# Kernel tuning notes

Hardware: AMD Instinct MI355X
Metric: run time of the kernel (lower is better)

## Reference

```python
import jax, jax.numpy as jnp
import numpy as np

HEADS = 8
DIM_HEAD = 64
EPS_NORM = 1e-5

def chan_layer_norm(x, g, b):
    # normalize over channel dim (axis=1), biased variance, eps inside sqrt
    mean = jnp.mean(x, axis=1, keepdims=True)
    var = jnp.mean((x - mean) ** 2, axis=1, keepdims=True)
    return (x - mean) / jnp.sqrt(var + EPS_NORM) * g + b

def l2norm(x):
    # F.normalize over dim=1 with eps=1e-12
    n = jnp.linalg.norm(x, axis=1, keepdims=True)
    return x / jnp.maximum(n, 1e-12)

def conv1x1(w, x):
    # w: (out_c, in_c), x: (b, in_c, h, w)
    return jnp.einsum('oc,bchw->bohw', w, x)

def setup_inputs() -> dict:
    key = jax.random.key(0)
    ks = jax.random.split(key, 8)
    dim, inner = 256, HEADS * DIM_HEAD
    B, H, W = 8, 64, 64
    inp = {
        'query_source': jax.random.normal(ks[0], (B, dim, H, W), jnp.float32),
        'context': jax.random.normal(ks[1], (B, dim, H, W), jnp.float32),
        'cn_g': jnp.ones((1, dim, 1, 1), jnp.float32),
        'cn_b': jnp.zeros((1, dim, 1, 1), jnp.float32),
        'qn_g': jnp.ones((1, dim, 1, 1), jnp.float32),
        'qn_b': jnp.zeros((1, dim, 1, 1), jnp.float32),
        'on_g': jnp.ones((1, dim, 1, 1), jnp.float32),
        'on_b': jnp.zeros((1, dim, 1, 1), jnp.float32),
        'w_kv': jax.random.normal(ks[2], (inner * 2, dim), jnp.float32) * (dim ** -0.5),
        'w_q': jax.random.normal(ks[3], (inner, dim), jnp.float32) * (dim ** -0.5),
        'w_out': jax.random.normal(ks[4], (dim, inner), jnp.float32) * (inner ** -0.5),
        'gamma': jnp.full((1,), 0.5, jnp.float32),  # nonzero so output depends on attention path
    }
    return inp

def reference(query_source, context, cn_g, cn_b, qn_g, qn_b, on_g, on_b, w_kv, w_q, w_out, gamma):
    B, C, Hq, Wq = query_source.shape
    _, _, Hc, Wc = context.shape
    kh = int(Hc ** 0.5)  # height_top_k default
    kw = int(Wc ** 0.5)  # width_top_k default

    ctx = chan_layer_norm(context, cn_g, cn_b)
    qs = chan_layer_norm(query_source, qn_g, qn_b)

    kv = conv1x1(w_kv, ctx)                      # (B, 2*inner, Hc, Wc)
    k, v = jnp.split(kv, 2, axis=1)
    q = conv1x1(w_q, qs)                         # (B, inner, Hq, Wq)

    def fold(x):
        b, hc, h, w = x.shape
        return x.reshape(b, HEADS, DIM_HEAD, h, w).reshape(b * HEADS, DIM_HEAD, h, w)
    q, k, v = fold(q), fold(k), fold(v)

    q, k = l2norm(q), l2norm(k)

    if kh < Hc or kw < Wc:
        k_abs = jnp.abs(k)
        q_probe = q.sum(axis=(2, 3))             # (bh, c)
        if kh < Hc:
            score_r = jnp.einsum('bc,bch->bh', q_probe, k_abs.sum(axis=3))
            idx_h = jax.lax.top_k(score_r, kh)[1]            # (bh, kh)
            idx = idx_h[:, None, :, None]
            k = jnp.take_along_axis(k, idx, axis=2)
            v = jnp.take_along_axis(v, idx, axis=2)
        if kw < Wc:
            score_c = jnp.einsum('bc,bcw->bw', q_probe, k_abs.sum(axis=2))
            idx_w = jax.lax.top_k(score_c, kw)[1]            # (bh, kw)
            idx = idx_w[:, None, None, :]
            k = jnp.take_along_axis(k, idx, axis=3)
            v = jnp.take_along_axis(v, idx, axis=3)

    def flat(x):  # (bh, c, h, w) -> (bh, h*w, c)
        bh, c = x.shape[:2]
        return x.reshape(bh, c, -1).transpose(0, 2, 1)
    qf, kf, vf = flat(q), flat(k), flat(v)

    sim = jnp.einsum('bid,bjd->bij', qf, kf)     # (bh, Hq*Wq, kh*kw)
    attn = jax.nn.softmax(sim, axis=-1)
    out = jnp.einsum('bij,bjd->bid', attn, vf)   # (bh, Hq*Wq, c)

    out = out.reshape(B, HEADS, Hq, Wq, DIM_HEAD)
    out = out.transpose(0, 1, 4, 2, 3).reshape(B, HEADS * DIM_HEAD, Hq, Wq)
    out = conv1x1(w_out, out)
    out = chan_layer_norm(out, on_g, on_b)
    return gamma * out + query_source
```

## Files before the change

kernel.cpp:

```cpp
#include <hip/hip_runtime.h>
#include <hip/hip_bf16.h>

#define BB 8
#define CDIM 256
#define PP 4096
#define NHEADS 8
#define DHEAD 64
#define INNER 512
#define NBH 64

using bf16 = __hip_bfloat16;
typedef short short8 __attribute__((ext_vector_type(8)));
typedef float f32x4 __attribute__((ext_vector_type(4)));
typedef unsigned short u16;

__device__ __forceinline__ float b2f(bf16 x) { return __bfloat162float(x); }
__device__ __forceinline__ bf16 f2b(float x) { return __float2bfloat16(x); }

__device__ __forceinline__ u16 f2h(float x) {
    union { float f; unsigned u; } c; c.f = x;
    unsigned r = c.u + 0x7FFF + ((c.u >> 16) & 1);
    return (u16)(r >> 16);
}
__device__ __forceinline__ float h2f(u16 h) {
    union { float f; unsigned u; } c; c.u = ((unsigned)h) << 16;
    return c.f;
}

__device__ __forceinline__ int sw(int row, int kb) {
    return row * 128 + (kb ^ ((row & 7) << 4));
}

__device__ __forceinline__ void gload16(const void* g, void* lds) {
    __builtin_amdgcn_global_load_lds((const __attribute__((address_space(1))) void*)g,
                                     (__attribute__((address_space(3))) void*)lds, 16, 0, 0);
}

__device__ __forceinline__ void remap(int& o0, int& p0, int& b) {
    unsigned GS = gridDim.x;
    unsigned h = (blockIdx.z * gridDim.y + blockIdx.y) * GS + blockIdx.x;
    unsigned xc = h & 7, m = h >> 3;
    unsigned g = (m / GS) * 8 + xc;
    o0 = (int)(m % GS) * 64;
    p0 = (int)(g & 63) * 64;
    b  = (int)(g >> 6);
}

__global__ __launch_bounds__(256) void wsplit_kernel(const float* __restrict__ W,
                                                     u16* __restrict__ WH,
                                                     u16* __restrict__ WL) {
    int i = blockIdx.x * 256 + threadIdx.x;
    float v = W[i];
    u16 hb = f2h(v);
    WH[i] = hb;
    if (WL) WL[i] = f2h(v - h2f(hb));
}

__global__ __launch_bounds__(256) void ln_split_kernel(const float* __restrict__ x,
                                                       const float* __restrict__ g,
                                                       const float* __restrict__ bb,
                                                       u16* __restrict__ XH,
                                                       u16* __restrict__ XL) {
    int b = blockIdx.y;
    int p0 = blockIdx.x * 64;
    int tid = threadIdx.x;
    int px = tid & 63, cg = tid >> 6;
    __shared__ float red_s[4][64], red_q[4][64], meanv[64], rstdv[64];

    const float* xb = x + (size_t)b * CDIM * PP + p0 + px;
    float s = 0.f, sq = 0.f;
#pragma unroll 8
    for (int i = 0; i < 64; ++i) {
        float v = xb[(size_t)(cg * 64 + i) * PP];
        s += v; sq += v * v;
    }
    red_s[cg][px] = s; red_q[cg][px] = sq;
    __syncthreads();
    if (tid < 64) {
        float ts = red_s[0][tid] + red_s[1][tid] + red_s[2][tid] + red_s[3][tid];
        float tq = red_q[0][tid] + red_q[1][tid] + red_q[2][tid] + red_q[3][tid];
        float mean = ts * (1.f / CDIM);
        float var  = tq * (1.f / CDIM) - mean * mean;
        meanv[tid] = mean;
        rstdv[tid] = rsqrtf(var + 1e-5f);
    }
    __syncthreads();
    float mean = meanv[px], rstd = rstdv[px];
    size_t orow = ((size_t)b * PP + p0 + px) * CDIM;
    for (int c0 = cg * 64; c0 < cg * 64 + 64; c0 += 8) {
        short8 hv, lv;
#pragma unroll
        for (int j = 0; j < 8; ++j) {
            int c = c0 + j;
            float v = xb[(size_t)c * PP];
            float n = (v - mean) * rstd * g[c] + bb[c];
            u16 hb = f2h(n);
            hv[j] = (short)hb;
            lv[j] = (short)f2h(n - h2f(hb));
        }
        *(short8*)(XH + orow + c0) = hv;
        *(short8*)(XL + orow + c0) = lv;
    }
}

__global__ __launch_bounds__(256) void mfma_qkv_kernel(const u16* __restrict__ WH,
                                                       const u16* __restrict__ WL,
                                                       const u16* __restrict__ XH,
                                                       const u16* __restrict__ XL,
                                                       u16* __restrict__ dstA,
                                                       u16* __restrict__ dstB,
                                                       int Kdim, int norm_below, int mode,
                                                       float* __restrict__ part_out,
                                                       const float* __restrict__ q_probe) {
    __shared__ alignas(16) char sm[32768];
    __shared__ float red[16][64];
    __shared__ float rinv[64];
    __shared__ float qp_s[64];
    char* AH = sm;
    char* AL = sm + 8192;
    char* BH = sm + 16384;
    char* BL = sm + 24576;
    float* C = (float*)sm;

    int o0, p0, b;
    remap(o0, p0, b);
    int tid = threadIdx.x;
    int l = tid & 63, w = tid >> 6;
    int wm = w >> 1, wn = w & 1;
    int lr = l & 15, lk = l >> 4;
    int r8 = l >> 3;
    int kswz = ((l & 7) * 16) ^ (r8 << 4);

    bool donorm = (o0 < norm_below);
    if (mode == 0 && donorm && tid < 64)
        qp_s[tid] = q_probe[(size_t)(b * NHEADS + (o0 >> 6)) * 64 + tid];

    f32x4 acc[2][2] = {};

    for (int k0 = 0; k0 < Kdim; k0 += 64) {
#pragma unroll
        for (int j = 0; j < 2; ++j) {
            int rb = w * 16 + j * 8;
            int row = rb + r8;
            size_t aoff = ((size_t)(o0 + row) * Kdim + k0) * 2 + kswz;
            size_t boff = (((size_t)b * PP + p0 + row) * Kdim + k0) * 2 + kswz;
            gload16((const char*)WH + aoff, AH + rb * 128);
            gload16((const char*)WL + aoff, AL + rb * 128);
            gload16((const char*)XH + boff, BH + rb * 128);
            gload16((const char*)XL + boff, BL + rb * 128);
        }
        __syncthreads();
#pragma unroll
        for (int kk = 0; kk < 2; ++kk) {
            int kb = kk * 64 + lk * 16;
            short8 ah[2], al[2], bh[2], bl[2];
#pragma unroll
            for (int f = 0; f < 2; ++f) {
                ah[f] = *(short8*)(AH + sw(wm * 32 + f * 16 + lr, kb));
                al[f] = *(short8*)(AL + sw(wm * 32 + f * 16 + lr, kb));
                bh[f] = *(short8*)(BH + sw(wn * 32 + f * 16 + lr, kb));
                bl[f] = *(short8*)(BL + sw(wn * 32 + f * 16 + lr, kb));
            }
#pragma unroll
            for (int fm = 0; fm < 2; ++fm)
#pragma unroll
                for (int fn = 0; fn < 2; ++fn) {
                    acc[fm][fn] = __builtin_amdgcn_mfma_f32_16x16x32_bf16(ah[fm], bh[fn], acc[fm][fn], 0, 0, 0);
                    acc[fm][fn] = __builtin_amdgcn_mfma_f32_16x16x32_bf16(ah[fm], bl[fn], acc[fm][fn], 0, 0, 0);
                    acc[fm][fn] = __builtin_amdgcn_mfma_f32_16x16x32_bf16(al[fm], bh[fn], acc[fm][fn], 0, 0, 0);
                }
        }
        __syncthreads();
    }

#pragma unroll
    for (int fm = 0; fm < 2; ++fm)
#pragma unroll
        for (int fn = 0; fn < 2; ++fn)
#pragma unroll
            for (int r = 0; r < 4; ++r)
                C[(wm * 32 + fm * 16 + lk * 4 + r) * 65 + wn * 32 + fn * 16 + lr] = acc[fm][fn][r];
    __syncthreads();

    int tx = tid & 15, ty = tid >> 4;
    float a2[4][4];
#pragma unroll
    for (int i = 0; i < 4; ++i)
#pragma unroll
        for (int j = 0; j < 4; ++j)
            a2[i][j] = C[(ty * 4 + i) * 65 + tx * 4 + j];

    if (donorm) {
#pragma unroll
        for (int j = 0; j < 4; ++j) {
            float sj = 0.f;
#pragma unroll
            for (int i = 0; i < 4; ++i) sj += a2[i][j] * a2[i][j];
            red[ty][tx * 4 + j] = sj;
        }
        __syncthreads();
        if (tid < 64) {
            float s = 0.f;
#pragma unroll
            for (int yy = 0; yy < 16; ++yy) s += red[yy][tid];
            rinv[tid] = 1.f / fmaxf(sqrtf(s), 1e-12f);
        }
        __syncthreads();
#pragma unroll
        for (int i = 0; i < 4; ++i)
#pragma unroll
            for (int j = 0; j < 4; ++j)
                a2[i][j] *= rinv[tx * 4 + j];
    }

    if (mode == 1) {
        int p_l = tid & 63, og = tid >> 6;
        float rv = rinv[p_l];
        u16* qrow = dstA + ((size_t)(b * NHEADS + (o0 >> 6)) * PP + p0 + p_l) * 64 + og * 16;
        short8 s0, s1;
#pragma unroll
        for (int i = 0; i < 8; ++i) s0[i] = (short)f2h(C[(og * 16 + i) * 65 + p_l] * rv);
#pragma unroll
        for (int i = 0; i < 8; ++i) s1[i] = (short)f2h(C[(og * 16 + 8 + i) * 65 + p_l] * rv);
        *(short8*)qrow = s0;
        *(short8*)(qrow + 8) = s1;
    } else {
        int oo = donorm ? o0 : (o0 - norm_below);
        u16* dest = donorm ? dstA : dstB;
#pragma unroll
        for (int i = 0; i < 4; ++i) {
            int oc = oo + ty * 4 + i;
            int bh = b * NHEADS + (oc >> 6);
            int d  = oc & 63;
            u16* drow = dest + ((size_t)bh * DHEAD + d) * PP + p0;
#pragma unroll
            for (int j = 0; j < 4; ++j) drow[tx * 4 + j] = f2h(a2[i][j]);
        }
    }

    if (donorm) {
        int bh = b * NHEADS + (o0 >> 6);
        int h  = p0 >> 6;
        if (mode == 0) {
            float cj[4];
#pragma unroll
            for (int j = 0; j < 4; ++j) {
                float s = 0.f;
#pragma unroll
                for (int i = 0; i < 4; ++i) s += qp_s[ty * 4 + i] * fabsf(a2[i][j]);
                cj[j] = s;
            }
            __syncthreads();
#pragma unroll
            for (int j = 0; j < 4; ++j) red[ty][tx * 4 + j] = cj[j];
            __syncthreads();
            if (tid < 64) {
                float s = 0.f;
#pragma unroll
                for (int t = 0; t < 16; ++t) s += red[t][tid];
                part_out[((size_t)bh * 64 + h) * 64 + tid] = s;
            }
        } else {
            float part[4];
#pragma unroll
            for (int i = 0; i < 4; ++i) {
                float s = 0.f;
#pragma unroll
                for (int j = 0; j < 4; ++j) s += a2[i][j];
                part[i] = s;
            }
            __syncthreads();
#pragma unroll
            for (int i = 0; i < 4; ++i) red[tx][ty * 4 + i] = part[i];
            __syncthreads();
            if (tid < 64) {
                float s = 0.f;
#pragma unroll
                for (int t = 0; t < 16; ++t) s += red[t][tid];
                part_out[((size_t)bh * 64 + h) * 64 + tid] = s;
            }
        }
    }
}

__global__ __launch_bounds__(64) void qreduce_kernel(const float* __restrict__ part,
                                                     float* __restrict__ q_probe) {
    int bh = blockIdx.x, d = threadIdx.x;
    float s = 0.f;
    for (int h = 0; h < 64; ++h) s += part[((size_t)bh * 64 + h) * 64 + d];
    q_probe[(size_t)bh * 64 + d] = s;
}

__global__ __launch_bounds__(256) void select_gather_kernel(const float* __restrict__ colpart,
                                                            const u16* __restrict__ kn,
                                                            const u16* __restrict__ vs,
                                                            u16* __restrict__ k_sel,
                                                            u16* __restrict__ v_selt) {
    int bh = blockIdx.x;
    int tid = threadIdx.x;
    __shared__ float M[64][65];
    __shared__ int selh[8], selw[8];
    for (int i = tid; i < 4096; i += 256) M[i >> 6][i & 63] = colpart[(size_t)bh * 4096 + i];
    __syncthreads();
    if (tid < 128) {
        int isCol = tid >> 6;
        int x = tid & 63;
        float sv = 0.f;
        if (isCol) { for (int h = 0; h < 64; ++h) sv += M[h][x]; }
        else       { for (int w = 0; w < 64; ++w) sv += M[x][w]; }
        float v = sv;
        for (int it = 0; it < 8; ++it) {
            float bv = v; int bi = x;
#pragma unroll
            for (int off = 32; off; off >>= 1) {
                float ov = __shfl_xor(bv, off);
                int   oi = __shfl_xor(bi, off);
                if (ov > bv || (ov == bv && oi < bi)) { bv = ov; bi = oi; }
            }
            if (x == 0) { if (isCol) selw[it] = bi; else selh[it] = bi; }
            if (x == bi) v = -3.4e38f;
        }
    }
    __syncthreads();
    for (int idx = tid; idx < 4096; idx += 256) {
        int j = idx >> 6, d = idx & 63;
        int p = selh[j >> 3] * 64 + selw[j & 7];
        u16 kv = kn[((size_t)bh * 64 + d) * PP + p];
        u16 vv = vs[((size_t)bh * 64 + d) * PP + p];
        k_sel[(size_t)bh * 4096 + j * 64 + d]  = kv;
        v_selt[(size_t)bh * 4096 + d * 64 + j] = vv;
    }
}

__global__ __launch_bounds__(256) void attn_mfma_kernel(const u16* __restrict__ qt,
                                                        const u16* __restrict__ ksel,
                                                        const u16* __restrict__ vselt,
                                                        u16* __restrict__ attn_t) {
    __shared__ alignas(16) char AQ[8192];
    __shared__ alignas(16) char BK[8192];
    __shared__ alignas(16) char BV[8192];
    __shared__ float SIM[64 * 68];
    int bh = blockIdx.y;
    int p0 = blockIdx.x * 64;
    int b = bh >> 3, h = bh & 7;
    int tid = threadIdx.x;
    int l = tid & 63, w = tid >> 6;
    int wm = w >> 1, wn = w & 1;
    int lr = l & 15, lk = l >> 4;
    int r8 = l >> 3;
    int kswz = ((l & 7) * 16) ^ (r8 << 4);

#pragma unroll
    for (int j = 0; j < 2; ++j) {
        int rb = w * 16 + j * 8;
        int row = rb + r8;
        gload16((const char*)qt + ((size_t)bh * PP + p0 + row) * 128 + kswz, AQ + rb * 128);
        gload16((const char*)ksel + ((size_t)bh * 64 + row) * 128 + kswz, BK + rb * 128);
        gload16((const char*)vselt + ((size_t)bh * 64 + row) * 128 + kswz, BV + rb * 128);
    }
    __syncthreads();

    f32x4 acc[2][2] = {};
#pragma unroll
    for (int kk = 0; kk < 2; ++kk) {
        int kb = kk * 64 + lk * 16;
        short8 av[2], bv[2];
#pragma unroll
        for (int f = 0; f < 2; ++f) {
            av[f] = *(short8*)(AQ + sw(wm * 32 + f * 16 + lr, kb));
            bv[f] = *(short8*)(BK + sw(wn * 32 + f * 16 + lr, kb));
        }
#pragma unroll
        for (int fm = 0; fm < 2; ++fm)
#pragma unroll
            for (int fn = 0; fn < 2; ++fn)
                acc[fm][fn] = __builtin_amdgcn_mfma_f32_16x16x32_bf16(av[fm], bv[fn], acc[fm][fn], 0, 0, 0);
    }
#pragma unroll
    for (int fm = 0; fm < 2; ++fm)
#pragma unroll
        for (int fn = 0; fn < 2; ++fn)
#pragma unroll
            for (int r = 0; r < 4; ++r)
                SIM[(wm * 32 + fm * 16 + lk * 4 + r) * 68 + wn * 32 + fn * 16 + lr] = acc[fm][fn][r];
    __syncthreads();

    {
        int p = tid >> 2, qd = tid & 3;
        const float* srow = &SIM[p * 68 + qd * 16];
        float v[16];
#pragma unroll
        for (int jj = 0; jj < 16; ++jj) v[jj] = srow[jj];
        float m = v[0];
#pragma unroll
        for (int jj = 1; jj < 16; ++jj) m = fmaxf(m, v[jj]);
        m = fmaxf(m, __shfl_xor(m, 1));
        m = fmaxf(m, __shfl_xor(m, 2));
        float s = 0.f;
#pragma unroll
        for (int jj = 0; jj < 16; ++jj) { v[jj] = __expf(v[jj] - m); s += v[jj]; }
        s += __shfl_xor(s, 1);
        s += __shfl_xor(s, 2);
        float rl = 1.f / s;
        short8 h0, h1;
#pragma unroll
        for (int jj = 0; jj < 8; ++jj) {
            h0[jj] = (short)f2h(v[jj] * rl);
            h1[jj] = (short)f2h(v[8 + jj] * rl);
        }
        *(short8*)(AQ + sw(p, qd * 32)) = h0;
        *(short8*)(AQ + sw(p, qd * 32 + 16)) = h1;
    }
    __syncthreads();

    f32x4 acc2[2][2] = {};
#pragma unroll
    for (int kk = 0; kk < 2; ++kk) {
        int kb = kk * 64 + lk * 16;
        short8 av[2], bv[2];
#pragma unroll
        for (int f = 0; f < 2; ++f) {
            av[f] = *(short8*)(AQ + sw(wm * 32 + f * 16 + lr, kb));
            bv[f] = *(short8*)(BV + sw(wn * 32 + f * 16 + lr, kb));
        }
#pragma unroll
        for (int fm = 0; fm < 2; ++fm)
#pragma unroll
            for (int fn = 0; fn < 2; ++fn)
                acc2[fm][fn] = __builtin_amdgcn_mfma_f32_16x16x32_bf16(av[fm], bv[fn], acc2[fm][fn], 0, 0, 0);
    }
    u16* ob = attn_t + ((size_t)b * PP + p0) * INNER + h * 64;
#pragma unroll
    for (int fm = 0; fm < 2; ++fm)
#pragma unroll
        for (int fn = 0; fn < 2; ++fn)
#pragma unroll
            for (int r = 0; r < 4; ++r)
                ob[(size_t)(wm * 32 + fm * 16 + lk * 4 + r) * INNER + wn * 32 + fn * 16 + lr]
                    = f2h(acc2[fm][fn][r]);
}

__global__ __launch_bounds__(256) void mfma_out_kernel(const u16* __restrict__ WHp,
                                                       const u16* __restrict__ Xt,
                                                       float* __restrict__ Y) {
    __shared__ alignas(16) char sm[16384];
    char* AH = sm;
    char* BH = sm + 8192;

    int o0, p0, b;
    remap(o0, p0, b);
    int tid = threadIdx.x;
    int l = tid & 63, w = tid >> 6;
    int wm = w >> 1, wn = w & 1;
    int lr = l & 15, lk = l >> 4;
    int r8 = l >> 3;
    int kswz = ((l & 7) * 16) ^ (r8 << 4);

    f32x4 acc[2][2] = {};

    for (int k0 = 0; k0 < INNER; k0 += 64) {
#pragma unroll
        for (int j = 0; j < 2; ++j) {
            int rb = w * 16 + j * 8;
            int row = rb + r8;
            size_t aoff = ((size_t)(o0 + row) * INNER + k0) * 2 + kswz;
            size_t boff = (((size_t)b * PP + p0 + row) * INNER + k0) * 2 + kswz;
            gload16((const char*)WHp + aoff, AH + rb * 128);
            gload16((const char*)Xt + boff, BH + rb * 128);
        }
        __syncthreads();
#pragma unroll
        for (int kk = 0; kk < 2; ++kk) {
            int kb = kk * 64 + lk * 16;
            short8 ah[2], bh[2];
#pragma unroll
            for (int f = 0; f < 2; ++f) {
                ah[f] = *(short8*)(AH + sw(wm * 32 + f * 16 + lr, kb));
                bh[f] = *(short8*)(BH + sw(wn * 32 + f * 16 + lr, kb));
            }
#pragma unroll
            for (int fm = 0; fm < 2; ++fm)
#pragma unroll
                for (int fn = 0; fn < 2; ++fn)
                    acc[fm][fn] = __builtin_amdgcn_mfma_f32_16x16x32_bf16(ah[fm], bh[fn], acc[fm][fn], 0, 0, 0);
        }
        __syncthreads();
    }
#pragma unroll
    for (int fm = 0; fm < 2; ++fm)
#pragma unroll
        for (int fn = 0; fn < 2; ++fn)
#pragma unroll
            for (int r = 0; r < 4; ++r)
                Y[((size_t)b * CDIM + o0 + wm * 32 + fm * 16 + lk * 4 + r) * PP
                  + p0 + wn * 32 + fn * 16 + lr] = acc[fm][fn][r];
}

__global__ __launch_bounds__(256) void final_ln_kernel(const float* __restrict__ y,
                                                       const float* __restrict__ g,
                                                       const float* __restrict__ bb,
                                                       const float* __restrict__ gamma,
                                                       const float* __restrict__ resid,
                                                       float* __restrict__ out) {
    int b = blockIdx.y;
    int p = blockIdx.x * 256 + threadIdx.x;
    const float* yb = y + (size_t)b * CDIM * PP + p;
    float s = 0.f, sq = 0.f;
    for (int c = 0; c < CDIM; ++c) {
        float v = yb[(size_t)c * PP];
        s += v; sq += v * v;
    }
    float mean = s * (1.f / CDIM);
    float var  = sq * (1.f / CDIM) - mean * mean;
    float rstd = rsqrtf(var + 1e-5f);
    float gm = gamma[0];
    const float* rb = resid + (size_t)b * CDIM * PP + p;
    float* ob = out + (size_t)b * CDIM * PP + p;
    for (int c = 0; c < CDIM; ++c) {
        float v = yb[(size_t)c * PP];
        float xn = (v - mean) * rstd * g[c] + bb[c];
        ob[(size_t)c * PP] = gm * xn + rb[(size_t)c * PP];
    }
}

extern "C" void kernel_launch(void* const* d_in, const int* in_sizes, int n_in,
                              void* d_out, int out_size, void* d_ws, size_t ws_size,
                              hipStream_t stream) {
    const float* query_source = (const float*)d_in[0];
    const float* context      = (const float*)d_in[1];
    const float* cn_g = (const float*)d_in[2];
    const float* cn_b = (const float*)d_in[3];
    const float* qn_g = (const float*)d_in[4];
    const float* qn_b = (const float*)d_in[5];
    const float* on_g = (const float*)d_in[6];
    const float* on_b = (const float*)d_in[7];
    const float* w_kv = (const float*)d_in[8];
    const float* w_q  = (const float*)d_in[9];
    const float* w_out= (const float*)d_in[10];
    const float* gamma= (const float*)d_in[11];
    float* out = (float*)d_out;

    char* ws = (char*)d_ws;
    u16*  XHt    = (u16*)(ws + 0);
    u16*  XLt    = (u16*)(ws + 16777216);
    u16*  attn_t = (u16*)(ws + 0);
    u16*   k_n  = (u16*)(ws + 33554432);
    float* y    = (float*)(ws + 33554432);
    u16*   v_s  = (u16*)(ws + 67108864);
    u16*   q_t  = (u16*)(ws + 100663296);
    u16*  WqH   = (u16*)(ws + 134217728);
    u16*  WqL   = (u16*)(ws + 134742016);
    u16*  k_sel = (u16*)(ws + 134217728);
    u16*  v_selt= (u16*)(ws + 134742016);
    u16*  WkvH  = (u16*)(ws + 135266304);
    u16*  WkvL  = (u16*)(ws + 135790592);
    u16*  WoutH = (u16*)(ws + 135266304);
    float* qprobe_part   = (float*)(ws + 136314880);
    float* colscore_part = (float*)(ws + 136314880);
    float* q_probe       = (float*)(ws + 137363456);

    dim3 blk(256);
    wsplit_kernel<<<dim3(512), blk, 0, stream>>>(w_q, WqH, WqL);
    ln_split_kernel<<<dim3(64, BB), blk, 0, stream>>>(query_source, qn_g, qn_b, XHt, XLt);
    mfma_qkv_kernel<<<dim3(8, 64, BB), blk, 0, stream>>>(WqH, WqL, XHt, XLt, q_t, nullptr,
                                                         CDIM, 512, 1, qprobe_part, nullptr);
    qreduce_kernel<<<dim3(64), dim3(64), 0, stream>>>(qprobe_part, q_probe);
    wsplit_kernel<<<dim3(1024), blk, 0, stream>>>(w_kv, WkvH, WkvL);
    ln_split_kernel<<<dim3(64, BB), blk, 0, stream>>>(context, cn_g, cn_b, XHt, XLt);
    mfma_qkv_kernel<<<dim3(16, 64, BB), blk, 0, stream>>>(WkvH, WkvL, XHt, XLt, k_n, v_s,
                                                          CDIM, 512, 0, colscore_part, q_probe);
    select_gather_kernel<<<dim3(64), blk, 0, stream>>>(colscore_part, k_n, v_s, k_sel, v_selt);
    wsplit_kernel<<<dim3(512), blk, 0, stream>>>(w_out, WoutH, nullptr);
    attn_mfma_kernel<<<dim3(64, NBH), blk, 0, stream>>>(q_t, k_sel, v_selt, attn_t);
    mfma_out_kernel<<<dim3(4, 64, BB), blk, 0, stream>>>(WoutH, attn_t, y);
    final_ln_kernel<<<dim3(16, BB), blk, 0, stream>>>(y, on_g, on_b, gamma, query_source, out);
}
```

Measured before the change: 390.9 us.

## Drop split-bf16 for V projection, double-buffer out GEMM, merge weight splits

```diff
diff --git a/kernel.cpp b/kernel.cpp
--- a/kernel.cpp
+++ b/kernel.cpp
@@ -11,6 +11,7 @@
 
 using bf16 = __hip_bfloat16;
 typedef short short8 __attribute__((ext_vector_type(8)));
+typedef short short4v __attribute__((ext_vector_type(4)));
 typedef float f32x4 __attribute__((ext_vector_type(4)));
 typedef unsigned short u16;
 
@@ -46,14 +47,25 @@
     b  = (int)(g >> 6);
 }
 
-__global__ __launch_bounds__(256) void wsplit_kernel(const float* __restrict__ W,
-                                                     u16* __restrict__ WH,
-                                                     u16* __restrict__ WL) {
+__global__ __launch_bounds__(256) void split2_kernel(const float* __restrict__ Wkv,
+                                                     const float* __restrict__ Wq,
+                                                     u16* __restrict__ KH, u16* __restrict__ KL,
+                                                     u16* __restrict__ QH, u16* __restrict__ QL) {
     int i = blockIdx.x * 256 + threadIdx.x;
-    float v = W[i];
-    u16 hb = f2h(v);
-    WH[i] = hb;
-    if (WL) WL[i] = f2h(v - h2f(hb));
+    if (i < 262144) {
+        float v = Wkv[i]; u16 hb = f2h(v);
+        KH[i] = hb; KL[i] = f2h(v - h2f(hb));
+    } else {
+        int j = i - 262144;
+        float v = Wq[j]; u16 hb = f2h(v);
+        QH[j] = hb; QL[j] = f2h(v - h2f(hb));
+    }
+}
+
+__global__ __launch_bounds__(256) void wsplit_hi_kernel(const float* __restrict__ W,
+                                                        u16* __restrict__ WH) {
+    int i = blockIdx.x * 256 + threadIdx.x;
+    WH[i] = f2h(W[i]);
 }
 
 __global__ __launch_bounds__(256) void ln_split_kernel(const float* __restrict__ x,
@@ -132,6 +144,7 @@
     int kswz = ((l & 7) * 16) ^ (r8 << 4);
 
     bool donorm = (o0 < norm_below);
+    bool lite = (mode == 0) && !donorm;
     if (mode == 0 && donorm && tid < 64)
         qp_s[tid] = q_probe[(size_t)(b * NHEADS + (o0 >> 6)) * 64 + tid];
 
@@ -145,30 +158,44 @@
             size_t aoff = ((size_t)(o0 + row) * Kdim + k0) * 2 + kswz;
             size_t boff = (((size_t)b * PP + p0 + row) * Kdim + k0) * 2 + kswz;
             gload16((const char*)WH + aoff, AH + rb * 128);
-            gload16((const char*)WL + aoff, AL + rb * 128);
             gload16((const char*)XH + boff, BH + rb * 128);
-            gload16((const char*)XL + boff, BL + rb * 128);
+            if (!lite) {
+                gload16((const char*)WL + aoff, AL + rb * 128);
+                gload16((const char*)XL + boff, BL + rb * 128);
+            }
         }
         __syncthreads();
 #pragma unroll
         for (int kk = 0; kk < 2; ++kk) {
             int kb = kk * 64 + lk * 16;
-            short8 ah[2], al[2], bh[2], bl[2];
+            short8 ah[2], bh[2];
 #pragma unroll
             for (int f = 0; f < 2; ++f) {
                 ah[f] = *(short8*)(AH + sw(wm * 32 + f * 16 + lr, kb));
-                al[f] = *(short8*)(AL + sw(wm * 32 + f * 16 + lr, kb));
                 bh[f] = *(short8*)(BH + sw(wn * 32 + f * 16 + lr, kb));
-                bl[f] = *(short8*)(BL + sw(wn * 32 + f * 16 + lr, kb));
-            }
-#pragma unroll
-            for (int fm = 0; fm < 2; ++fm)
-#pragma unroll
-                for (int fn = 0; fn < 2; ++fn) {
-                    acc[fm][fn] = __builtin_amdgcn_mfma_f32_16x16x32_bf16(ah[fm], bh[fn], acc[fm][fn], 0, 0, 0);
-                    acc[fm][fn] = __builtin_amdgcn_mfma_f32_16x16x32_bf16(ah[fm], bl[fn], acc[fm][fn], 0, 0, 0);
-                    acc[fm][fn] = __builtin_amdgcn_mfma_f32_16x16x32_bf16(al[fm], bh[fn], acc[fm][fn], 0, 0, 0);
+            }
+            if (!lite) {
+                short8 al[2], bl[2];
+#pragma unroll
+                for (int f = 0; f < 2; ++f) {
+                    al[f] = *(short8*)(AL + sw(wm * 32 + f * 16 + lr, kb));
+                    bl[f] = *(short8*)(BL + sw(wn * 32 + f * 16 + lr, kb));
                 }
+#pragma unroll
+                for (int fm = 0; fm < 2; ++fm)
+#pragma unroll
+                    for (int fn = 0; fn < 2; ++fn) {
+                        acc[fm][fn] = __builtin_amdgcn_mfma_f32_16x16x32_bf16(ah[fm], bh[fn], acc[fm][fn], 0, 0, 0);
+                        acc[fm][fn] = __builtin_amdgcn_mfma_f32_16x16x32_bf16(ah[fm], bl[fn], acc[fm][fn], 0, 0, 0);
+                        acc[fm][fn] = __builtin_amdgcn_mfma_f32_16x16x32_bf16(al[fm], bh[fn], acc[fm][fn], 0, 0, 0);
+                    }
+            } else {
+#pragma unroll
+                for (int fm = 0; fm < 2; ++fm)
+#pragma unroll
+                    for (int fn = 0; fn < 2; ++fn)
+                        acc[fm][fn] = __builtin_amdgcn_mfma_f32_16x16x32_bf16(ah[fm], bh[fn], acc[fm][fn], 0, 0, 0);
+            }
         }
         __syncthreads();
     }
@@ -233,8 +260,10 @@
             int bh = b * NHEADS + (oc >> 6);
             int d  = oc & 63;
             u16* drow = dest + ((size_t)bh * DHEAD + d) * PP + p0;
-#pragma unroll
-            for (int j = 0; j < 4; ++j) drow[tx * 4 + j] = f2h(a2[i][j]);
+            short4v pk;
+#pragma unroll
+            for (int j = 0; j < 4; ++j) pk[j] = (short)f2h(a2[i][j]);
+            *(short4v*)(drow + tx * 4) = pk;
         }
     }
 
@@ -443,9 +472,7 @@
 __global__ __launch_bounds__(256) void mfma_out_kernel(const u16* __restrict__ WHp,
                                                        const u16* __restrict__ Xt,
                                                        float* __restrict__ Y) {
-    __shared__ alignas(16) char sm[16384];
-    char* AH = sm;
-    char* BH = sm + 8192;
+    __shared__ alignas(16) char sm[32768];
 
     int o0, p0, b;
     remap(o0, p0, b);
@@ -458,17 +485,26 @@
 
     f32x4 acc[2][2] = {};
 
-    for (int k0 = 0; k0 < INNER; k0 += 64) {
+    auto STAGE = [&](int bufi, int k0) {
+        char* base = sm + bufi * 16384;
 #pragma unroll
         for (int j = 0; j < 2; ++j) {
             int rb = w * 16 + j * 8;
             int row = rb + r8;
             size_t aoff = ((size_t)(o0 + row) * INNER + k0) * 2 + kswz;
             size_t boff = (((size_t)b * PP + p0 + row) * INNER + k0) * 2 + kswz;
-            gload16((const char*)WHp + aoff, AH + rb * 128);
-            gload16((const char*)Xt + boff, BH + rb * 128);
-        }
-        __syncthreads();
+            gload16((const char*)WHp + aoff, base + rb * 128);
+            gload16((const char*)Xt + boff, base + 8192 + rb * 128);
+        }
+    };
+
+    STAGE(0, 0);
+    __syncthreads();
+    int cur = 0;
+    for (int t = 0; t < 8; ++t) {
+        if (t < 7) STAGE(cur ^ 1, (t + 1) * 64);
+        char* AH = sm + cur * 16384;
+        char* BH = AH + 8192;
 #pragma unroll
         for (int kk = 0; kk < 2; ++kk) {
             int kb = kk * 64 + lk * 16;
@@ -485,6 +521,7 @@
                     acc[fm][fn] = __builtin_amdgcn_mfma_f32_16x16x32_bf16(ah[fm], bh[fn], acc[fm][fn], 0, 0, 0);
         }
         __syncthreads();
+        cur ^= 1;
     }
 #pragma unroll
     for (int fm = 0; fm < 2; ++fm)
@@ -560,17 +597,16 @@
     float* q_probe       = (float*)(ws + 137363456);
 
     dim3 blk(256);
-    wsplit_kernel<<<dim3(512), blk, 0, stream>>>(w_q, WqH, WqL);
+    split2_kernel<<<dim3(1536), blk, 0, stream>>>(w_kv, w_q, WkvH, WkvL, WqH, WqL);
     ln_split_kernel<<<dim3(64, BB), blk, 0, stream>>>(query_source, qn_g, qn_b, XHt, XLt);
     mfma_qkv_kernel<<<dim3(8, 64, BB), blk, 0, stream>>>(WqH, WqL, XHt, XLt, q_t, nullptr,
                                                          CDIM, 512, 1, qprobe_part, nullptr);
     qreduce_kernel<<<dim3(64), dim3(64), 0, stream>>>(qprobe_part, q_probe);
-    wsplit_kernel<<<dim3(1024), blk, 0, stream>>>(w_kv, WkvH, WkvL);
     ln_split_kernel<<<dim3(64, BB), blk, 0, stream>>>(context, cn_g, cn_b, XHt, XLt);
     mfma_qkv_kernel<<<dim3(16, 64, BB), blk, 0, stream>>>(WkvH, WkvL, XHt, XLt, k_n, v_s,
                                                           CDIM, 512, 0, colscore_part, q_probe);
     select_gather_kernel<<<dim3(64), blk, 0, stream>>>(colscore_part, k_n, v_s, k_sel, v_selt);
-    wsplit_kernel<<<dim3(512), blk, 0, stream>>>(w_out, WoutH, nullptr);
+    wsplit_hi_kernel<<<dim3(512), blk, 0, stream>>>(w_out, WoutH);
     attn_mfma_kernel<<<dim3(64, NBH), blk, 0, stream>>>(q_t, k_sel, v_selt, attn_t);
     mfma_out_kernel<<<dim3(4, 64, BB), blk, 0, stream>>>(WoutH, attn_t, y);
     final_ln_kernel<<<dim3(16, BB), blk, 0, stream>>>(y, on_g, on_b, gamma, query_source, out);
```

Result: faster. 383.1 us (-2.0%).
